# Kernel tuning notes

Hardware: AMD Instinct MI355X
Metric: run time of the kernel (lower is better)

## Reference

```python
import jax, jax.numpy as jnp
import numpy as np

N_NODES = 50000
N_EDGES = 800000
D_FEAT = 128
HIDDEN = 96
N_CLASSES = 10
N_GRAPHS = 64


def setup_inputs() -> dict:
    key = jax.random.key(0)
    ks = jax.random.split(key, 12)
    x = jax.random.normal(ks[0], (N_NODES, D_FEAT), dtype=jnp.float32)
    edge_index = jax.random.randint(ks[1], (2, N_EDGES), 0, N_NODES, dtype=jnp.int64)
    batch = jnp.sort(jax.random.randint(ks[2], (N_NODES,), 0, N_GRAPHS, dtype=jnp.int64))
    def glorot(k, fan_in, fan_out):
        s = jnp.sqrt(6.0 / (fan_in + fan_out)).astype(jnp.float32)
        return jax.random.uniform(k, (fan_in, fan_out), jnp.float32, -s, s)
    return {
        "x": x,
        "edge_index": edge_index,
        "batch": batch,
        "W1": glorot(ks[3], D_FEAT, HIDDEN), "b1": jnp.zeros((HIDDEN,), jnp.float32),
        "W2": glorot(ks[4], HIDDEN, HIDDEN), "b2": jnp.zeros((HIDDEN,), jnp.float32),
        "W3": glorot(ks[5], HIDDEN, HIDDEN), "b3": jnp.zeros((HIDDEN,), jnp.float32),
        "lw1": glorot(ks[6], HIDDEN, HIDDEN), "lb1": jnp.zeros((HIDDEN,), jnp.float32),
        "lw2": glorot(ks[7], HIDDEN, N_CLASSES), "lb2": jnp.zeros((N_CLASSES,), jnp.float32),
    }


def reference(x, edge_index, batch, W1, b1, W2, b2, W3, b3, lw1, lb1, lw2, lb2):
    N = x.shape[0]
    # --- GCN normalization with self-loops (D^-1/2 (A+I) D^-1/2) ---
    loop = jnp.arange(N, dtype=edge_index.dtype)
    src = jnp.concatenate([edge_index[0], loop])  # [E+N]
    dst = jnp.concatenate([edge_index[1], loop])  # [E+N]
    deg = jax.ops.segment_sum(jnp.ones_like(dst, dtype=x.dtype), dst, num_segments=N)
    dinv = jax.lax.rsqrt(deg)  # deg >= 1 thanks to self-loops
    norm = (dinv[src] * dinv[dst])[:, None]  # [E+N, 1]

    def gcn_conv(h, W, b):
        hw = h @ W                                    # [N, H] transform first (smaller dim)
        msg = hw[src] * norm                          # gather + scale, [E+N, H]
        agg = jax.ops.segment_sum(msg, dst, num_segments=N)  # scatter-add, [N, H]
        return agg + b

    h = jax.nn.relu(gcn_conv(x, W1, b1))
    h = jax.nn.relu(gcn_conv(h, W2, b2))
    h = jax.nn.relu(gcn_conv(h, W3, b3))

    # --- global mean pool over graphs ---
    sums = jax.ops.segment_sum(h, batch, num_segments=N_GRAPHS)          # [G, H]
    cnts = jax.ops.segment_sum(jnp.ones((N,), h.dtype), batch, num_segments=N_GRAPHS)
    pooled = sums / jnp.maximum(cnts, 1.0)[:, None]

    # --- MLP head (dropout is identity in eval mode) ---
    z = jax.nn.relu(pooled @ lw1 + lb1)
    return z @ lw2 + lb2
```

## Files before the change

### kernel.cpp

```cpp
#include <hip/hip_runtime.h>
#include <hip/hip_fp16.h>

#define N_NODES 50000
#define N_EDGES 800000
#define D_FEAT 128
#define HIDDEN 96
#define N_CLASSES 10
#define N_GRAPHS 64
#define POOL_SLICES 16
#define SCAN_BLOCKS ((N_NODES + 255) / 256)

union F4H8 { float4 f; __half2 h[4]; };

typedef __attribute__((ext_vector_type(8))) _Float16 half8;
typedef __attribute__((ext_vector_type(4))) float f32x4;


__global__ void k_init(int* __restrict__ deg_i, float* __restrict__ pooled) {
    int i = blockIdx.x * 256 + threadIdx.x;
    if (i < N_NODES) deg_i[i] = 0;
    if (i < N_GRAPHS * HIDDEN) pooled[i] = 0.f;
}

__global__ void k_deg(const int* __restrict__ dst, int* __restrict__ deg_i,
                      int* __restrict__ rank) {
    int e = blockIdx.x * 256 + threadIdx.x;
    if (e < N_EDGES) rank[e] = atomicAdd(&deg_i[dst[e]], 1);
}

__global__ __launch_bounds__(256) void k_partial(const int* __restrict__ deg_i,
                                                 int* __restrict__ bsum) {
    __shared__ int wsum[4];
    int i = blockIdx.x * 256 + threadIdx.x;
    int v = (i < N_NODES) ? deg_i[i] : 0;
    for (int o = 32; o > 0; o >>= 1) v += __shfl_down(v, o, 64);
    int lane = threadIdx.x & 63, wid = threadIdx.x >> 6;
    if (lane == 0) wsum[wid] = v;
    __syncthreads();
    if (threadIdx.x == 0) bsum[blockIdx.x] = wsum[0] + wsum[1] + wsum[2] + wsum[3];
}

__global__ __launch_bounds__(256) void k_scanblk(const int* __restrict__ bsum,
                                                 int* __restrict__ bpre) {
    __shared__ int s[256];
    int t = threadIdx.x;
    s[t] = (t < SCAN_BLOCKS) ? bsum[t] : 0;
    __syncthreads();
    for (int off = 1; off < 256; off <<= 1) {
        int v = s[t];
        int a = (t >= off) ? s[t - off] : 0;
        __syncthreads();
        s[t] = v + a;
        __syncthreads();
    }
    if (t <= SCAN_BLOCKS) bpre[t] = (t == 0) ? 0 : s[t - 1];
}

__global__ __launch_bounds__(256) void k_offs(const int* __restrict__ deg_i,
                                              const int* __restrict__ bpre,
                                              int* __restrict__ offs,
                                              float* __restrict__ dinv) {
    __shared__ int s[256];
    int t = threadIdx.x;
    int i = blockIdx.x * 256 + t;
    int d = (i < N_NODES) ? deg_i[i] : 0;
    s[t] = d;
    __syncthreads();
    for (int off = 1; off < 256; off <<= 1) {
        int v = s[t];
        int a = (t >= off) ? s[t - off] : 0;
        __syncthreads();
        s[t] = v + a;
        __syncthreads();
    }
    int incl = s[t];
    int excl = incl - d;
    if (i < N_NODES) {
        int o = bpre[blockIdx.x] + excl;
        offs[i] = o;
        dinv[i] = rsqrtf((float)(d + 1));
        if (i == N_NODES - 1) offs[N_NODES] = o + d;
    }
}

__global__ void k_fill(const int* __restrict__ src, const int* __restrict__ dst,
                       const int* __restrict__ rank, const int* __restrict__ offs,
                       int* __restrict__ csr_src) {
    int e = blockIdx.x * 256 + threadIdx.x;
    if (e >= N_EDGES) return;
    csr_src[offs[dst[e]] + rank[e]] = src[e];
}


template <int K, bool F32IN>
__global__ __launch_bounds__(256) void k_mm_mfma(const void* __restrict__ hin,
                                                 const float* __restrict__ W,
                                                 const float* __restrict__ dinv,
                                                 __half* __restrict__ hws) {
    constexpr int CH = K / 8;
    constexpr int KSTEPS = K / 32;
    __shared__ float4 Hl[64 * 16];
    __shared__ float4 Wt[96 * 16];
    int t = threadIdx.x;
    int base = blockIdx.x * 64;

    _Float16* WtH = (_Float16*)Wt;
    for (int idx = t; idx < K * 96; idx += 256) {
        int k = idx / 96, f = idx % 96;
        int kc = k >> 3, ke = k & 7;
        WtH[(f * 16 + (kc ^ (f & 15))) * 8 + ke] = (_Float16)W[idx];
    }
    if (F32IN) {
        const float4* x4 = (const float4*)hin;
        for (int idx = t; idx < 64 * CH; idx += 256) {
            int row = idx / CH, c = idx % CH;
            int gr = base + row; if (gr >= N_NODES) gr = N_NODES - 1;
            float4 a = x4[(size_t)gr * (CH * 2) + c * 2];
            float4 b = x4[(size_t)gr * (CH * 2) + c * 2 + 1];
            F4H8 o;
            o.h[0] = __floats2half2_rn(a.x, a.y);
            o.h[1] = __floats2half2_rn(a.z, a.w);
            o.h[2] = __floats2half2_rn(b.x, b.y);
            o.h[3] = __floats2half2_rn(b.z, b.w);
            Hl[row * 16 + (c ^ (row & 15))] = o.f;
        }
    } else {
        const float4* h4 = (const float4*)hin;
        for (int idx = t; idx < 64 * CH; idx += 256) {
            int row = idx / CH, c = idx % CH;
            int gr = base + row; if (gr >= N_NODES) gr = N_NODES - 1;
            Hl[row * 16 + (c ^ (row & 15))] = h4[(size_t)gr * CH + c];
        }
    }
    __syncthreads();

    int w = t >> 6, l = t & 63;
    int lr = l & 15, lq = l >> 4;
    int arow = w * 16 + lr;
    f32x4 acc[6];
    #pragma unroll
    for (int i = 0; i < 6; ++i) acc[i] = (f32x4){0.f, 0.f, 0.f, 0.f};

    #pragma unroll
    for (int ks = 0; ks < KSTEPS; ++ks) {
        int ck = ks * 4 + lq;
        half8 a = *(const half8*)&Hl[arow * 16 + (ck ^ lr)];
        #pragma unroll
        for (int tf = 0; tf < 6; ++tf) {
            int f = tf * 16 + lr;
            half8 b = *(const half8*)&Wt[f * 16 + (ck ^ lr)];
            acc[tf] = __builtin_amdgcn_mfma_f32_16x16x32_f16(a, b, acc[tf], 0, 0, 0);
        }
    }

    float dv[4];
    #pragma unroll
    for (int j = 0; j < 4; ++j) {
        int n = base + w * 16 + lq * 4 + j;
        if (n >= N_NODES) n = N_NODES - 1;
        dv[j] = dinv[n];
    }
    __syncthreads();
    _Float16* C = (_Float16*)Hl;
    #pragma unroll
    for (int tf = 0; tf < 6; ++tf)
        #pragma unroll
        for (int j = 0; j < 4; ++j)
            C[(w * 16 + lq * 4 + j) * 96 + tf * 16 + lr] =
                (_Float16)(acc[tf][j] * dv[j]);
    __syncthreads();
    const float4* C4 = (const float4*)C;
    for (int idx = t; idx < 64 * 12; idx += 256) {
        int row = idx / 12;
        int n = base + row;
        if (n < N_NODES)
            ((float4*)hws)[(size_t)n * 12 + (idx % 12)] = C4[idx];
    }
}


__global__ __launch_bounds__(256) void k_agg(const __half* __restrict__ hws,
                                             const float* __restrict__ dinv,
                                             const int* __restrict__ offs,
                                             const int* __restrict__ csr_src,
                                             const float* __restrict__ bias,
                                             __half* __restrict__ hout) {
    int id = blockIdx.x * 256 + threadIdx.x;
    if (id >= N_NODES * 12) return;
    int c = id % 12;
    int n = id / 12;
    const float4* hw4 = (const float4*)hws;
    F4H8 v;
    v.f = hw4[(size_t)n * 12 + c];
    float2 p0 = __half22float2(v.h[0]), p1 = __half22float2(v.h[1]);
    float2 p2 = __half22float2(v.h[2]), p3 = __half22float2(v.h[3]);
    float4 A = make_float4(p0.x, p0.y, p1.x, p1.y);
    float4 B = make_float4(p2.x, p2.y, p3.x, p3.y);

    int beg = offs[n], end = offs[n + 1];
    int i = beg;
    for (; i + 2 <= end; i += 2) {
        F4H8 v0, v1;
        v0.f = hw4[(size_t)csr_src[i] * 12 + c];
        v1.f = hw4[(size_t)csr_src[i + 1] * 12 + c];
        float2 a0 = __half22float2(v0.h[0]), a1 = __half22float2(v0.h[1]);
        float2 a2 = __half22float2(v0.h[2]), a3 = __half22float2(v0.h[3]);
        float2 b0 = __half22float2(v1.h[0]), b1 = __half22float2(v1.h[1]);
        float2 b2 = __half22float2(v1.h[2]), b3 = __half22float2(v1.h[3]);
        A.x += a0.x + b0.x; A.y += a0.y + b0.y;
        A.z += a1.x + b1.x; A.w += a1.y + b1.y;
        B.x += a2.x + b2.x; B.y += a2.y + b2.y;
        B.z += a3.x + b3.x; B.w += a3.y + b3.y;
    }
    if (i < end) {
        F4H8 v0;
        v0.f = hw4[(size_t)csr_src[i] * 12 + c];
        float2 a0 = __half22float2(v0.h[0]), a1 = __half22float2(v0.h[1]);
        float2 a2 = __half22float2(v0.h[2]), a3 = __half22float2(v0.h[3]);
        A.x += a0.x; A.y += a0.y; A.z += a1.x; A.w += a1.y;
        B.x += a2.x; B.y += a2.y; B.z += a3.x; B.w += a3.y;
    }

    float di = dinv[n];
    float4 b0 = ((const float4*)bias)[c * 2];
    float4 b1 = ((const float4*)bias)[c * 2 + 1];
    A.x = fmaxf(A.x * di + b0.x, 0.f); A.y = fmaxf(A.y * di + b0.y, 0.f);
    A.z = fmaxf(A.z * di + b0.z, 0.f); A.w = fmaxf(A.w * di + b0.w, 0.f);
    B.x = fmaxf(B.x * di + b1.x, 0.f); B.y = fmaxf(B.y * di + b1.y, 0.f);
    B.z = fmaxf(B.z * di + b1.z, 0.f); B.w = fmaxf(B.w * di + b1.w, 0.f);

    F4H8 o;
    o.h[0] = __floats2half2_rn(A.x, A.y);
    o.h[1] = __floats2half2_rn(A.z, A.w);
    o.h[2] = __floats2half2_rn(B.x, B.y);
    o.h[3] = __floats2half2_rn(B.z, B.w);
    ((float4*)hout)[(size_t)n * 12 + c] = o.f;
}


__global__ __launch_bounds__(192) void k_pool(const __half* __restrict__ h,
                                              const int* __restrict__ batch,
                                              float* __restrict__ pooled) {
    int g = blockIdx.x / POOL_SLICES;
    int slice = blockIdx.x % POOL_SLICES;
    int t = threadIdx.x;
    int f = t % HIDDEN;
    int j = t / HIDDEN;
    int lo = 0, hi = N_NODES;
    while (lo < hi) { int m = (lo + hi) >> 1; if (batch[m] < g) lo = m + 1; else hi = m; }
    int start = lo;
    hi = N_NODES;
    while (lo < hi) { int m = (lo + hi) >> 1; if (batch[m] < g + 1) lo = m + 1; else hi = m; }
    int end = lo;
    int len = end - start;
    int per = (len + POOL_SLICES - 1) / POOL_SLICES;
    int s0 = start + slice * per;
    int s1 = min(s0 + per, end);
    float acc = 0.f;
    for (int n = s0 + j; n < s1; n += 2) acc += __half2float(h[(size_t)n * HIDDEN + f]);
    atomicAdd(&pooled[g * HIDDEN + f], acc);
}


__global__ __launch_bounds__(128) void k_head_mlp(const float* __restrict__ pooled_in,
                                                  const int* __restrict__ batch,
                                                  const float* __restrict__ lw1,
                                                  const float* __restrict__ lb1,
                                                  const float* __restrict__ lw2,
                                                  const float* __restrict__ lb2,
                                                  float* __restrict__ out) {
    __shared__ float pooled[HIDDEN];
    __shared__ float zbuf[HIDDEN];
    int g = blockIdx.x;
    int t = threadIdx.x;
    int lo = 0, hi = N_NODES;
    while (lo < hi) { int m = (lo + hi) >> 1; if (batch[m] < g) lo = m + 1; else hi = m; }
    int start = lo;
    hi = N_NODES;
    while (lo < hi) { int m = (lo + hi) >> 1; if (batch[m] < g + 1) lo = m + 1; else hi = m; }
    int end = lo;
    float cnt = fmaxf((float)(end - start), 1.f);
    if (t < HIDDEN) pooled[t] = pooled_in[g * HIDDEN + t] / cnt;
    __syncthreads();
    if (t < HIDDEN) {
        float a = lb1[t];
        for (int k = 0; k < HIDDEN; ++k) a += pooled[k] * lw1[k * HIDDEN + t];
        zbuf[t] = fmaxf(a, 0.f);
    }
    __syncthreads();
    if (t < N_CLASSES) {
        float a = lb2[t];
        for (int k = 0; k < HIDDEN; ++k) a += zbuf[k] * lw2[k * N_CLASSES + t];
        out[g * N_CLASSES + t] = a;
    }
}


extern "C" void kernel_launch(void* const* d_in, const int* in_sizes, int n_in,
                              void* d_out, int out_size, void* d_ws, size_t ws_size,
                              hipStream_t stream) {
    const float* x   = (const float*)d_in[0];
    const int*   ei  = (const int*)d_in[1];
    const int*   bat = (const int*)d_in[2];
    const float* W1  = (const float*)d_in[3];
    const float* b1  = (const float*)d_in[4];
    const float* W2  = (const float*)d_in[5];
    const float* b2  = (const float*)d_in[6];
    const float* W3  = (const float*)d_in[7];
    const float* b3  = (const float*)d_in[8];
    const float* lw1 = (const float*)d_in[9];
    const float* lb1 = (const float*)d_in[10];
    const float* lw2 = (const float*)d_in[11];
    const float* lb2 = (const float*)d_in[12];
    float* out = (float*)d_out;

    const int* src = ei;
    const int* dst = ei + N_EDGES;

    char* ws = (char*)d_ws;
    size_t off = 0;
    auto alloc = [&](size_t bytes) {
        size_t p = off;
        off = (off + bytes + 255) & ~(size_t)255;
        return p;
    };
    float*  dinv    = (float*) (ws + alloc(sizeof(float) * N_NODES));
    int*    deg_i   = (int*)   (ws + alloc(sizeof(int) * N_NODES));
    int*    offs    = (int*)   (ws + alloc(sizeof(int) * (N_NODES + 1)));
    int*    bsum    = (int*)   (ws + alloc(sizeof(int) * (SCAN_BLOCKS + 1)));
    int*    bpre    = (int*)   (ws + alloc(sizeof(int) * (SCAN_BLOCKS + 1)));
    int*    rank    = (int*)   (ws + alloc(sizeof(int) * N_EDGES));
    int*    csr_src = (int*)   (ws + alloc(sizeof(int) * N_EDGES));
    __half* bufA    = (__half*)(ws + alloc(sizeof(__half) * (size_t)N_NODES * HIDDEN));
    __half* bufB    = (__half*)(ws + alloc(sizeof(__half) * (size_t)N_NODES * HIDDEN));
    float*  pooled  = (float*) (ws + alloc(sizeof(float) * N_GRAPHS * HIDDEN));
    (void)ws_size;

    const int nodeBlocks = (N_NODES + 255) / 256;
    const int edgeBlocks = (N_EDGES + 255) / 256;
    const int mmBlocks   = (N_NODES + 63) / 64;
    const int aggBlocks  = (N_NODES * 12 + 255) / 256;

    k_init<<<nodeBlocks, 256, 0, stream>>>(deg_i, pooled);
    k_deg<<<edgeBlocks, 256, 0, stream>>>(dst, deg_i, rank);
    k_partial<<<SCAN_BLOCKS, 256, 0, stream>>>(deg_i, bsum);
    k_scanblk<<<1, 256, 0, stream>>>(bsum, bpre);
    k_offs<<<SCAN_BLOCKS, 256, 0, stream>>>(deg_i, bpre, offs, dinv);
    k_fill<<<edgeBlocks, 256, 0, stream>>>(src, dst, rank, offs, csr_src);

    k_mm_mfma<D_FEAT, true><<<mmBlocks, 256, 0, stream>>>(x, W1, dinv, bufA);
    k_agg<<<aggBlocks, 256, 0, stream>>>(bufA, dinv, offs, csr_src, b1, bufB);
    k_mm_mfma<HIDDEN, false><<<mmBlocks, 256, 0, stream>>>(bufB, W2, dinv, bufA);
    k_agg<<<aggBlocks, 256, 0, stream>>>(bufA, dinv, offs, csr_src, b2, bufB);
    k_mm_mfma<HIDDEN, false><<<mmBlocks, 256, 0, stream>>>(bufB, W3, dinv, bufA);
    k_agg<<<aggBlocks, 256, 0, stream>>>(bufA, dinv, offs, csr_src, b3, bufB);

    k_pool<<<N_GRAPHS * POOL_SLICES, 192, 0, stream>>>(bufB, bat, pooled);
    k_head_mlp<<<N_GRAPHS, 128, 0, stream>>>(pooled, bat, lw1, lb1, lw2, lb2, out);
}
```

Baseline: 215.5 us.

## Bucket nodes by in-degree and process aggregation in degree-sorted order

Result: slower. 485.0 us (+125.1%).

```diff
diff --git a/kernel.cpp b/kernel.cpp
--- a/kernel.cpp
+++ b/kernel.cpp
@@ -9,6 +9,7 @@
 #define N_GRAPHS 64
 #define POOL_SLICES 16
 #define SCAN_BLOCKS ((N_NODES + 255) / 256)
+#define NBUCKET 256
 
 union F4H8 { float4 f; __half2 h[4]; };
 
@@ -16,10 +17,12 @@
 typedef __attribute__((ext_vector_type(4))) float f32x4;
 
 
-__global__ void k_init(int* __restrict__ deg_i, float* __restrict__ pooled) {
+__global__ void k_init(int* __restrict__ deg_i, float* __restrict__ pooled,
+                       int* __restrict__ bcnt, int* __restrict__ bcur) {
     int i = blockIdx.x * 256 + threadIdx.x;
     if (i < N_NODES) deg_i[i] = 0;
     if (i < N_GRAPHS * HIDDEN) pooled[i] = 0.f;
+    if (i < NBUCKET) { bcnt[i] = 0; bcur[i] = 0; }
 }
 
 __global__ void k_deg(const int* __restrict__ dst, int* __restrict__ deg_i,
@@ -59,7 +62,8 @@
 __global__ __launch_bounds__(256) void k_offs(const int* __restrict__ deg_i,
                                               const int* __restrict__ bpre,
                                               int* __restrict__ offs,
-                                              float* __restrict__ dinv) {
+                                              float* __restrict__ dinv,
+                                              int* __restrict__ bcnt) {
     __shared__ int s[256];
     int t = threadIdx.x;
     int i = blockIdx.x * 256 + t;
@@ -80,7 +84,33 @@
         offs[i] = o;
         dinv[i] = rsqrtf((float)(d + 1));
         if (i == N_NODES - 1) offs[N_NODES] = o + d;
-    }
+        atomicAdd(&bcnt[d < NBUCKET - 1 ? d : NBUCKET - 1], 1);
+    }
+}
+
+__global__ __launch_bounds__(256) void k_bscan(const int* __restrict__ bcnt,
+                                               int* __restrict__ boff) {
+    __shared__ int s[NBUCKET];
+    int t = threadIdx.x;
+    s[t] = bcnt[t];
+    __syncthreads();
+    for (int off = 1; off < NBUCKET; off <<= 1) {
+        int v = s[t];
+        int a = (t >= off) ? s[t - off] : 0;
+        __syncthreads();
+        s[t] = v + a;
+        __syncthreads();
+    }
+    boff[t] = (t == 0) ? 0 : s[t - 1];
+}
+
+__global__ void k_bscatter(const int* __restrict__ deg_i, const int* __restrict__ boff,
+                           int* __restrict__ bcur, int* __restrict__ perm) {
+    int i = blockIdx.x * 256 + threadIdx.x;
+    if (i >= N_NODES) return;
+    int d = deg_i[i];
+    int b = d < NBUCKET - 1 ? d : NBUCKET - 1;
+    perm[boff[b] + atomicAdd(&bcur[b], 1)] = i;
 }
 
 __global__ void k_fill(const int* __restrict__ src, const int* __restrict__ dst,
@@ -183,12 +213,13 @@
                                              const float* __restrict__ dinv,
                                              const int* __restrict__ offs,
                                              const int* __restrict__ csr_src,
+                                             const int* __restrict__ perm,
                                              const float* __restrict__ bias,
                                              __half* __restrict__ hout) {
     int id = blockIdx.x * 256 + threadIdx.x;
     if (id >= N_NODES * 12) return;
     int c = id % 12;
-    int n = id / 12;
+    int n = perm[id / 12];
     const float4* hw4 = (const float4*)hws;
     F4H8 v;
     v.f = hw4[(size_t)n * 12 + c];
@@ -329,6 +360,10 @@
     int*    offs    = (int*)   (ws + alloc(sizeof(int) * (N_NODES + 1)));
     int*    bsum    = (int*)   (ws + alloc(sizeof(int) * (SCAN_BLOCKS + 1)));
     int*    bpre    = (int*)   (ws + alloc(sizeof(int) * (SCAN_BLOCKS + 1)));
+    int*    bcnt    = (int*)   (ws + alloc(sizeof(int) * NBUCKET));
+    int*    bcur    = (int*)   (ws + alloc(sizeof(int) * NBUCKET));
+    int*    boff    = (int*)   (ws + alloc(sizeof(int) * NBUCKET));
+    int*    perm    = (int*)   (ws + alloc(sizeof(int) * N_NODES));
     int*    rank    = (int*)   (ws + alloc(sizeof(int) * N_EDGES));
     int*    csr_src = (int*)   (ws + alloc(sizeof(int) * N_EDGES));
     __half* bufA    = (__half*)(ws + alloc(sizeof(__half) * (size_t)N_NODES * HIDDEN));
@@ -341,19 +376,21 @@
     const int mmBlocks   = (N_NODES + 63) / 64;
     const int aggBlocks  = (N_NODES * 12 + 255) / 256;
 
-    k_init<<<nodeBlocks, 256, 0, stream>>>(deg_i, pooled);
+    k_init<<<nodeBlocks, 256, 0, stream>>>(deg_i, pooled, bcnt, bcur);
     k_deg<<<edgeBlocks, 256, 0, stream>>>(dst, deg_i, rank);
     k_partial<<<SCAN_BLOCKS, 256, 0, stream>>>(deg_i, bsum);
     k_scanblk<<<1, 256, 0, stream>>>(bsum, bpre);
-    k_offs<<<SCAN_BLOCKS, 256, 0, stream>>>(deg_i, bpre, offs, dinv);
+    k_offs<<<SCAN_BLOCKS, 256, 0, stream>>>(deg_i, bpre, offs, dinv, bcnt);
+    k_bscan<<<1, NBUCKET, 0, stream>>>(bcnt, boff);
+    k_bscatter<<<nodeBlocks, 256, 0, stream>>>(deg_i, boff, bcur, perm);
     k_fill<<<edgeBlocks, 256, 0, stream>>>(src, dst, rank, offs, csr_src);
 
     k_mm_mfma<D_FEAT, true><<<mmBlocks, 256, 0, stream>>>(x, W1, dinv, bufA);
-    k_agg<<<aggBlocks, 256, 0, stream>>>(bufA, dinv, offs, csr_src, b1, bufB);
+    k_agg<<<aggBlocks, 256, 0, stream>>>(bufA, dinv, offs, csr_src, perm, b1, bufB);
     k_mm_mfma<HIDDEN, false><<<mmBlocks, 256, 0, stream>>>(bufB, W2, dinv, bufA);
-    k_agg<<<aggBlocks, 256, 0, stream>>>(bufA, dinv, offs, csr_src, b2, bufB);
+    k_agg<<<aggBlocks, 256, 0, stream>>>(bufA, dinv, offs, csr_src, perm, b2, bufB);
     k_mm_mfma<HIDDEN, false><<<mmBlocks, 256, 0, stream>>>(bufB, W3, dinv, bufA);
-    k_agg<<<aggBlocks, 256, 0, stream>>>(bufA, dinv, offs, csr_src, b3, bufB);
+    k_agg<<<aggBlocks, 256, 0, stream>>>(bufA, dinv, offs, csr_src, perm, b3, bufB);
 
     k_pool<<<N_GRAPHS * POOL_SLICES, 192, 0, stream>>>(bufB, bat, pooled);
     k_head_mlp<<<N_GRAPHS, 128, 0, stream>>>(pooled, bat, lw1, lb1, lw2, lb2, out);
```
